# Optimization experiments

Measured on AMD Instinct MI355X. Metric: run time of the kernel, lower is better.

## Reference

```python
import jax, jax.numpy as jnp
import numpy as np

E = 1024
H = 16
D = E // H
S = 2048
B = 2

def setup_inputs() -> dict:
    key = jax.random.key(0)
    ks = jax.random.split(key, 5)
    x = jax.random.normal(ks[0], (B, S, E), dtype=jnp.float32)
    W_qkv = jax.random.normal(ks[1], (E, 3 * E), dtype=jnp.float32) / np.sqrt(E)
    b_qkv = jax.random.normal(ks[2], (3 * E,), dtype=jnp.float32) * 0.02
    W_out = jax.random.normal(ks[3], (E, E), dtype=jnp.float32) / np.sqrt(E)
    b_out = jax.random.normal(ks[4], (E,), dtype=jnp.float32) * 0.02
    return {"x": x, "W_qkv": W_qkv, "b_qkv": b_qkv, "W_out": W_out, "b_out": b_out}

def reference(x, W_qkv, b_qkv, W_out, b_out):
    b, s, e = x.shape
    qkv = x @ W_qkv + b_qkv                      # [B,S,3E]
    q, k, v = jnp.split(qkv, 3, axis=-1)
    # [B,S,E] -> [B,H,S,D]
    q = q.reshape(b, s, H, D).transpose(0, 2, 1, 3)
    k = k.reshape(b, s, H, D).transpose(0, 2, 1, 3)
    v = v.reshape(b, s, H, D).transpose(0, 2, 1, 3)
    scale = 1.0 / np.sqrt(D)
    att = jnp.einsum('bhqd,bhkd->bhqk', q, k) * scale
    causal = jnp.tril(jnp.ones((s, s), dtype=bool))
    att = jnp.where(causal[None, None], att, -jnp.inf)
    att = jax.nn.softmax(att, axis=-1)
    out = jnp.einsum('bhqk,bhkd->bhqd', att, v)  # [B,H,S,D]
    out = out.transpose(0, 2, 1, 3).reshape(b, s, e)
    return out @ W_out + b_out
```

## Files before the change

kernel.cpp:

```cpp
#include <hip/hip_runtime.h>

typedef unsigned short u16;
typedef __bf16  bf16x8 __attribute__((ext_vector_type(8)));
typedef float   f32x4  __attribute__((ext_vector_type(4)));
typedef unsigned int   u32x4 __attribute__((ext_vector_type(4)));
typedef unsigned short u16x4 __attribute__((ext_vector_type(4)));
typedef unsigned short u16x8 __attribute__((ext_vector_type(8)));

#define BB 2
#define HH 16
#define DD 64
#define SS 2048
#define EE 1024

#define QSCALE 0.1803368801111244f

static __device__ __forceinline__ u16 f2bf(float f) {
    unsigned int u = __float_as_uint(f);
    u += 0x7FFFu + ((u >> 16) & 1u);
    return (u16)(u >> 16);
}

union BfCast { u32x4 u; bf16x8 b; };
static __device__ __forceinline__ bf16x8 ldb8(const u16* p) {
    BfCast x; x.u = *(const u32x4*)p; return x.b;
}

static __device__ __forceinline__ void gload16(const u16* g, u16* l) {
    __builtin_amdgcn_global_load_lds(
        (const __attribute__((address_space(1))) unsigned int*)g,
        (__attribute__((address_space(3))) unsigned int*)l, 16, 0, 0);
}

#define UG (32 * 512)
static __device__ __forceinline__ int kidx(int s, int d) {
    return (((s >> 4) * 2 + (d >> 5)) * 512) + ((((d >> 3) & 3) * 16 + (s & 15)) * 8) + (d & 7);
}
static __device__ __forceinline__ int vidx(int key, int d) {
    return (((key >> 5) * 4 + (d >> 4)) * 512) + ((((key >> 3) & 3) * 16 + (d & 15)) * 8) + (key & 7);
}

__global__ __launch_bounds__(256) void prep_kernel(
    const float* __restrict__ x,    u16* __restrict__ xb,
    const float* __restrict__ Wqkv, u16* __restrict__ wqkvT,
    const float* __restrict__ Wout, u16* __restrict__ woutT)
{
    __shared__ float tile[32][33];
    const int bid = blockIdx.x;
    if (bid < 2048) {
        const int t = bid * 256 + threadIdx.x;
        const int u = t >> 6, w = t & 63;
        const int m = (u >> 5) * 16 + (w & 15);
        const int k = (u & 31) * 32 + (w >> 4) * 8;
        const float* p = x + m * 1024 + k;
        const f32x4 a = *(const f32x4*)p;
        const f32x4 b = *(const f32x4*)(p + 4);
        u16x8 o;
        o[0] = f2bf(a[0]); o[1] = f2bf(a[1]); o[2] = f2bf(a[2]); o[3] = f2bf(a[3]);
        o[4] = f2bf(b[0]); o[5] = f2bf(b[1]); o[6] = f2bf(b[2]); o[7] = f2bf(b[3]);
        *(u16x8*)&xb[u * 512 + w * 8] = o;
        return;
    }
    const float* in; u16* out; int C, tb;
    if (bid < 2048 + 3072) { in = Wqkv; out = wqkvT; C = 3072; tb = bid - 2048; }
    else                   { in = Wout; out = woutT; C = 1024; tb = bid - 5120; }
    const int tx = threadIdx.x & 31;
    const int ty = threadIdx.x >> 5;
    const int ct = C >> 5;
    const int bc = tb % ct, br = tb / ct;
    const int c0 = bc * 32, r0 = br * 32;
    #pragma unroll
    for (int i = 0; i < 4; i++)
        tile[ty + i * 8][tx] = in[(r0 + ty + i * 8) * C + c0 + tx];
    __syncthreads();
    #pragma unroll
    for (int i = 0; i < 4; i++) {
        const int n = c0 + ty + i * 8;
        out[((n >> 4) * 32 + (r0 >> 5)) * 512 + (((tx >> 3) & 3) * 16 + (n & 15)) * 8 + (tx & 7)]
            = f2bf(tile[tx][ty + i * 8]);
    }
}

__global__ __launch_bounds__(256) void gemm_qkv_kernel(
    const u16* __restrict__ Af,
    const u16* __restrict__ Bf,
    const float* __restrict__ bias,
    u16* __restrict__ Qb, u16* __restrict__ Kb, u16* __restrict__ Vb)
{
    __shared__ __align__(16) u16 Us[2][16 * 512];
    const int lane = threadIdx.x & 63;
    const int wave = threadIdx.x >> 6;
    const int nb = 3 * EE / 128;
    const int tm = blockIdx.x / nb, tn = blockIdx.x % nb;
    const int lm = lane & 15, quad = lane >> 4;

    const u16* sp[4];
    #pragma unroll
    for (int j = 0; j < 4; j++) {
        const int idx = 4 * wave + j;
        sp[j] = (idx < 8) ? (Af + (tm * 8 + idx) * UG + lane * 8)
                          : (Bf + (tn * 8 + idx - 8) * UG + lane * 8);
    }
    u16* ld0 = &Us[0][4 * wave * 512];
    u16* ld1 = &Us[1][4 * wave * 512];

    const int wy = wave >> 1, wx = wave & 1;
    f32x4 acc[4][4] = {};

    #pragma unroll
    for (int j = 0; j < 4; j++) gload16(sp[j], ld0 + j * 512);

    for (int it = 0; it < 32; ++it) {
        const int cur = it & 1;
        __syncthreads();
        if (it + 1 < 32) {
            u16* ld = cur ? ld0 : ld1;
            const int ko = (it + 1) * 512;
            #pragma unroll
            for (int j = 0; j < 4; j++) gload16(sp[j] + ko, ld + j * 512);
        }
        bf16x8 af[4], bf[4];
        #pragma unroll
        for (int i = 0; i < 4; i++) {
            af[i] = ldb8(&Us[cur][(wy * 4 + i) * 512 + lane * 8]);
            bf[i] = ldb8(&Us[cur][(8 + wx * 4 + i) * 512 + lane * 8]);
        }
        #pragma unroll
        for (int mi = 0; mi < 4; mi++)
            #pragma unroll
            for (int ni = 0; ni < 4; ni++)
                acc[mi][ni] = __builtin_amdgcn_mfma_f32_16x16x32_bf16(af[mi], bf[ni], acc[mi][ni], 0, 0, 0);
    }

    const int gm0 = tm * 128 + wy * 64;
    const int gn0 = tn * 128 + wx * 64;
    #pragma unroll
    for (int ni = 0; ni < 4; ni++) {
        const int n = gn0 + ni * 16 + lm;
        const float bv = bias[n];
        const int which = n >> 10;
        const int e = n & 1023;
        const int h = e >> 6, d = e & 63;
        #pragma unroll
        for (int mi = 0; mi < 4; mi++) {
            if (which == 2) {
                const int m0 = gm0 + mi * 16 + quad * 4;
                const int b = m0 >> 11, key0 = m0 & 2047;
                u16x4 pk;
                #pragma unroll
                for (int r = 0; r < 4; r++) pk[r] = f2bf(acc[mi][ni][r] + bv);
                *(u16x4*)&Vb[(b * HH + h) * 131072 + vidx(key0, d)] = pk;
            } else if (which == 1) {
                #pragma unroll
                for (int r = 0; r < 4; r++) {
                    const int m = gm0 + mi * 16 + quad * 4 + r;
                    const int b = m >> 11, s = m & 2047;
                    Kb[(b * HH + h) * 131072 + kidx(s, d)] = f2bf(acc[mi][ni][r] + bv);
                }
            } else {
                #pragma unroll
                for (int r = 0; r < 4; r++) {
                    const int m = gm0 + mi * 16 + quad * 4 + r;
                    const int b = m >> 11, s = m & 2047;
                    Qb[((b * HH + h) * SS + s) * DD + d] = f2bf((acc[mi][ni][r] + bv) * QSCALE);
                }
            }
        }
    }
}

__global__ __launch_bounds__(256) void attn_kernel(
    const u16* __restrict__ Qb, const u16* __restrict__ Kb,
    const u16* __restrict__ Vb, u16* __restrict__ Ob)
{
    __shared__ __align__(16) u16 Ks[2][4096];
    __shared__ __align__(16) u16 Vs[2][4096];
    __shared__ __align__(16) u16 Plds[4 * 16 * 72];
    const int tid = threadIdx.x;
    const int lane = tid & 63, wave = tid >> 6;
    const int lm = lane & 15, quad = lane >> 4;
    const int bh = blockIdx.x & 31;
    const int qt = (SS / 64 - 1) - (blockIdx.x >> 5);
    const int q0 = qt * 64;
    const int qrow = q0 + wave * 16;
    const int b = bh >> 4, h = bh & 15;

    const u16* qbase = Qb + (bh * SS + qrow) * DD;
    const bf16x8 qf0 = ldb8(qbase + lm * DD + quad * 8);
    const bf16x8 qf1 = ldb8(qbase + lm * DD + 32 + quad * 8);

    const u16* ktile = Kb + bh * 131072;
    const u16* vtile = Vb + bh * 131072;
    u16* Pw = Plds + wave * (16 * 72);

    BfCast oc; oc.u = (u32x4){0x3F803F80u, 0x3F803F80u, 0x3F803F80u, 0x3F803F80u};
    const bf16x8 ones = oc.b;

    f32x4 oacc[4] = {};
    f32x4 lacc = {0.f, 0.f, 0.f, 0.f};

    const int ktmax = qt + 1;
    {
        const u16* kg = ktile + wave * 1024 + lane * 8;
        const u16* vg = vtile + wave * 1024 + lane * 8;
        gload16(kg,       &Ks[0][wave * 1024]);
        gload16(kg + 512, &Ks[0][wave * 1024 + 512]);
        gload16(vg,       &Vs[0][wave * 1024]);
        gload16(vg + 512, &Vs[0][wave * 1024 + 512]);
    }
    for (int kt = 0; kt < ktmax; ++kt) {
        const int cur = kt & 1;
        const int k0 = kt * 64;
        __syncthreads();
        if (kt + 1 < ktmax) {
            const u16* kg = ktile + (kt + 1) * 4096 + wave * 1024 + lane * 8;
            const u16* vg = vtile + (kt + 1) * 4096 + wave * 1024 + lane * 8;
            gload16(kg,       &Ks[cur ^ 1][wave * 1024]);
            gload16(kg + 512, &Ks[cur ^ 1][wave * 1024 + 512]);
            gload16(vg,       &Vs[cur ^ 1][wave * 1024]);
            gload16(vg + 512, &Vs[cur ^ 1][wave * 1024 + 512]);
        }

        f32x4 s[4];
        #pragma unroll
        for (int g = 0; g < 4; g++) {
            f32x4 z = {0.f, 0.f, 0.f, 0.f};
            z    = __builtin_amdgcn_mfma_f32_16x16x32_bf16(ldb8(&Ks[cur][(g * 2) * 512 + lane * 8]), qf0, z, 0, 0, 0);
            s[g] = __builtin_amdgcn_mfma_f32_16x16x32_bf16(ldb8(&Ks[cur][(g * 2 + 1) * 512 + lane * 8]), qf1, z, 0, 0, 0);
        }
        if (k0 + 63 > qrow) {
            const int lim = qrow + lm - k0 - quad * 4;
            #pragma unroll
            for (int g = 0; g < 4; g++)
                #pragma unroll
                for (int r = 0; r < 4; r++)
                    if (g * 16 + r > lim) s[g][r] = -INFINITY;
        }
        #pragma unroll
        for (int g = 0; g < 4; g++) {
            u16x4 pk;
            #pragma unroll
            for (int r = 0; r < 4; r++) pk[r] = f2bf(__builtin_amdgcn_exp2f(s[g][r]));
            *(u16x4*)&Pw[lm * 72 + g * 16 + quad * 4] = pk;
        }
        const bf16x8 pf0 = ldb8(&Pw[lm * 72 + quad * 8]);
        const bf16x8 pf1 = ldb8(&Pw[lm * 72 + 32 + quad * 8]);
        lacc = __builtin_amdgcn_mfma_f32_16x16x32_bf16(ones, pf0, lacc, 0, 0, 0);
        lacc = __builtin_amdgcn_mfma_f32_16x16x32_bf16(ones, pf1, lacc, 0, 0, 0);
        #pragma unroll
        for (int dg = 0; dg < 4; dg++) {
            oacc[dg] = __builtin_amdgcn_mfma_f32_16x16x32_bf16(ldb8(&Vs[cur][dg * 512 + lane * 8]), pf0, oacc[dg], 0, 0, 0);
            oacc[dg] = __builtin_amdgcn_mfma_f32_16x16x32_bf16(ldb8(&Vs[cur][(4 + dg) * 512 + lane * 8]), pf1, oacc[dg], 0, 0, 0);
        }
    }
    const float inv = 1.0f / lacc[0];
    u16* ob = Ob + (((b * SS + qrow) >> 4) * 32 + h * 2) * 512;
    #pragma unroll
    for (int dg = 0; dg < 4; dg++) {
        u16x4 pk;
        #pragma unroll
        for (int r = 0; r < 4; r++) pk[r] = f2bf(oacc[dg][r] * inv);
        *(u16x4*)&ob[(dg >> 1) * 512 + (((dg * 2 + (quad >> 1)) & 3) * 16 + lm) * 8 + (quad & 1) * 4] = pk;
    }
}

__global__ __launch_bounds__(256) void gemm_out_kernel(
    const u16* __restrict__ Af,
    const u16* __restrict__ Bf,
    const float* __restrict__ bias,
    float* __restrict__ Out)
{
    __shared__ __align__(16) u16 Us[2][16 * 512];
    const int lane = threadIdx.x & 63;
    const int wave = threadIdx.x >> 6;
    const int nb = EE / 128;
    const int tm = blockIdx.x / nb, tn = blockIdx.x % nb;
    const int lm = lane & 15, quad = lane >> 4;

    const u16* sp[4];
    #pragma unroll
    for (int j = 0; j < 4; j++) {
        const int idx = 4 * wave + j;
        sp[j] = (idx < 8) ? (Af + (tm * 8 + idx) * UG + lane * 8)
                          : (Bf + (tn * 8 + idx - 8) * UG + lane * 8);
    }
    u16* ld0 = &Us[0][4 * wave * 512];
    u16* ld1 = &Us[1][4 * wave * 512];

    const int wy = wave >> 1, wx = wave & 1;
    f32x4 acc[4][4] = {};

    #pragma unroll
    for (int j = 0; j < 4; j++) gload16(sp[j], ld0 + j * 512);

    for (int it = 0; it < 32; ++it) {
        const int cur = it & 1;
        __syncthreads();
        if (it + 1 < 32) {
            u16* ld = cur ? ld0 : ld1;
            const int ko = (it + 1) * 512;
            #pragma unroll
            for (int j = 0; j < 4; j++) gload16(sp[j] + ko, ld + j * 512);
        }
        bf16x8 af[4], bf[4];
        #pragma unroll
        for (int i = 0; i < 4; i++) {
            af[i] = ldb8(&Us[cur][(wy * 4 + i) * 512 + lane * 8]);
            bf[i] = ldb8(&Us[cur][(8 + wx * 4 + i) * 512 + lane * 8]);
        }
        #pragma unroll
        for (int mi = 0; mi < 4; mi++)
            #pragma unroll
            for (int ni = 0; ni < 4; ni++)
                acc[mi][ni] = __builtin_amdgcn_mfma_f32_16x16x32_bf16(af[mi], bf[ni], acc[mi][ni], 0, 0, 0);
    }

    const int gm0 = tm * 128 + wy * 64;
    const int gn0 = tn * 128 + wx * 64;
    #pragma unroll
    for (int ni = 0; ni < 4; ni++) {
        const int n = gn0 + ni * 16 + lm;
        const float bv = bias[n];
        #pragma unroll
        for (int mi = 0; mi < 4; mi++)
            #pragma unroll
            for (int r = 0; r < 4; r++)
                Out[(gm0 + mi * 16 + quad * 4 + r) * EE + n] = acc[mi][ni][r] + bv;
    }
}

extern "C" void kernel_launch(void* const* d_in, const int* in_sizes, int n_in,
                              void* d_out, int out_size, void* d_ws, size_t ws_size,
                              hipStream_t stream)
{
    const float* x     = (const float*)d_in[0];
    const float* Wqkv  = (const float*)d_in[1];
    const float* bqkv  = (const float*)d_in[2];
    const float* Wout  = (const float*)d_in[3];
    const float* bout  = (const float*)d_in[4];
    float* out = (float*)d_out;

    char* ws = (char*)d_ws;
    u16* xb    = (u16*)(ws + 0);
    u16* wqkvT = (u16*)(ws + 8388608);
    u16* woutT = (u16*)(ws + 14680064);
    u16* Qb    = (u16*)(ws + 16777216);
    u16* Kb    = (u16*)(ws + 25165824);
    u16* Vb    = (u16*)(ws + 33554432);
    u16* Ob    = (u16*)(ws + 41943040);
    if (ws_size < 50331648) return;

    prep_kernel<<<2048 + 3072 + 1024, 256, 0, stream>>>(x, xb, Wqkv, wqkvT, Wout, woutT);
    gemm_qkv_kernel<<<(BB * SS / 128) * (3 * EE / 128), 256, 0, stream>>>(xb, wqkvT, bqkv, Qb, Kb, Vb);
    attn_kernel<<<BB * HH * (SS / 64), 256, 0, stream>>>(Qb, Kb, Vb, Ob);
    gemm_out_kernel<<<(BB * SS / 128) * (EE / 128), 256, 0, stream>>>(Ob, woutT, bout, out);
}
```

Measured before the change: 171.9 us.

## Process 128 query rows per attention block, two 16-row fragments per wave

The attention kernel now gives each block 128 query rows instead of 64. Each wave owns 32 rows as two 16-row fragments that share the same K/V tiles staged in LDS. This halves the grid and the total global K/V traffic per query, and amortizes LDS loads and barriers over more compute. In exchange it uses more registers and launches fewer blocks (512), which may hurt occupancy and load balance on the causal triangle. Fully masked fragments are skipped per key tile.

```diff
diff --git a/kernel.cpp b/kernel.cpp
--- a/kernel.cpp
+++ b/kernel.cpp
@@ -180,14 +180,18 @@
     const int lane = tid & 63, wave = tid >> 6;
     const int lm = lane & 15, quad = lane >> 4;
     const int bh = blockIdx.x & 31;
-    const int qt = (SS / 64 - 1) - (blockIdx.x >> 5);
-    const int q0 = qt * 64;
-    const int qrow = q0 + wave * 16;
+    const int qt = (SS / 128 - 1) - (blockIdx.x >> 5);
+    const int q0 = qt * 128;
+    const int qrow = q0 + wave * 32;
     const int b = bh >> 4, h = bh & 15;
 
     const u16* qbase = Qb + (bh * SS + qrow) * DD;
-    const bf16x8 qf0 = ldb8(qbase + lm * DD + quad * 8);
-    const bf16x8 qf1 = ldb8(qbase + lm * DD + 32 + quad * 8);
+    bf16x8 qf[2][2];
+    #pragma unroll
+    for (int f = 0; f < 2; f++) {
+        qf[f][0] = ldb8(qbase + (f * 16 + lm) * DD + quad * 8);
+        qf[f][1] = ldb8(qbase + (f * 16 + lm) * DD + 32 + quad * 8);
+    }
 
     const u16* ktile = Kb + bh * 131072;
     const u16* vtile = Vb + bh * 131072;
@@ -196,10 +200,10 @@
     BfCast oc; oc.u = (u32x4){0x3F803F80u, 0x3F803F80u, 0x3F803F80u, 0x3F803F80u};
     const bf16x8 ones = oc.b;
 
-    f32x4 oacc[4] = {};
-    f32x4 lacc = {0.f, 0.f, 0.f, 0.f};
-
-    const int ktmax = qt + 1;
+    f32x4 oacc[2][4] = {};
+    f32x4 lacc[2] = {};
+
+    const int ktmax = qt * 2 + 2;
     {
         const u16* kg = ktile + wave * 1024 + lane * 8;
         const u16* vg = vtile + wave * 1024 + lane * 8;
@@ -221,46 +225,55 @@
             gload16(vg + 512, &Vs[cur ^ 1][wave * 1024 + 512]);
         }
 
-        f32x4 s[4];
-        #pragma unroll
-        for (int g = 0; g < 4; g++) {
-            f32x4 z = {0.f, 0.f, 0.f, 0.f};
-            z    = __builtin_amdgcn_mfma_f32_16x16x32_bf16(ldb8(&Ks[cur][(g * 2) * 512 + lane * 8]), qf0, z, 0, 0, 0);
-            s[g] = __builtin_amdgcn_mfma_f32_16x16x32_bf16(ldb8(&Ks[cur][(g * 2 + 1) * 512 + lane * 8]), qf1, z, 0, 0, 0);
-        }
-        if (k0 + 63 > qrow) {
-            const int lim = qrow + lm - k0 - quad * 4;
-            #pragma unroll
-            for (int g = 0; g < 4; g++)
-                #pragma unroll
-                for (int r = 0; r < 4; r++)
-                    if (g * 16 + r > lim) s[g][r] = -INFINITY;
-        }
-        #pragma unroll
-        for (int g = 0; g < 4; g++) {
+        #pragma unroll
+        for (int f = 0; f < 2; f++) {
+            const int qrf = qrow + f * 16;
+            if (k0 > qrf + 15) continue;
+
+            f32x4 s[4];
+            #pragma unroll
+            for (int g = 0; g < 4; g++) {
+                f32x4 z = {0.f, 0.f, 0.f, 0.f};
+                z    = __builtin_amdgcn_mfma_f32_16x16x32_bf16(ldb8(&Ks[cur][(g * 2) * 512 + lane * 8]), qf[f][0], z, 0, 0, 0);
+                s[g] = __builtin_amdgcn_mfma_f32_16x16x32_bf16(ldb8(&Ks[cur][(g * 2 + 1) * 512 + lane * 8]), qf[f][1], z, 0, 0, 0);
+            }
+            if (k0 + 63 > qrf) {
+                const int lim = qrf + lm - k0 - quad * 4;
+                #pragma unroll
+                for (int g = 0; g < 4; g++)
+                    #pragma unroll
+                    for (int r = 0; r < 4; r++)
+                        if (g * 16 + r > lim) s[g][r] = -INFINITY;
+            }
+            #pragma unroll
+            for (int g = 0; g < 4; g++) {
+                u16x4 pk;
+                #pragma unroll
+                for (int r = 0; r < 4; r++) pk[r] = f2bf(__builtin_amdgcn_exp2f(s[g][r]));
+                *(u16x4*)&Pw[lm * 72 + g * 16 + quad * 4] = pk;
+            }
+            const bf16x8 pf0 = ldb8(&Pw[lm * 72 + quad * 8]);
+            const bf16x8 pf1 = ldb8(&Pw[lm * 72 + 32 + quad * 8]);
+            lacc[f] = __builtin_amdgcn_mfma_f32_16x16x32_bf16(ones, pf0, lacc[f], 0, 0, 0);
+            lacc[f] = __builtin_amdgcn_mfma_f32_16x16x32_bf16(ones, pf1, lacc[f], 0, 0, 0);
+            #pragma unroll
+            for (int dg = 0; dg < 4; dg++) {
+                oacc[f][dg] = __builtin_amdgcn_mfma_f32_16x16x32_bf16(ldb8(&Vs[cur][dg * 512 + lane * 8]), pf0, oacc[f][dg], 0, 0, 0);
+                oacc[f][dg] = __builtin_amdgcn_mfma_f32_16x16x32_bf16(ldb8(&Vs[cur][(4 + dg) * 512 + lane * 8]), pf1, oacc[f][dg], 0, 0, 0);
+            }
+        }
+    }
+    #pragma unroll
+    for (int f = 0; f < 2; f++) {
+        const float inv = 1.0f / lacc[f][0];
+        u16* ob = Ob + (((b * SS + qrow + f * 16) >> 4) * 32 + h * 2) * 512;
+        #pragma unroll
+        for (int dg = 0; dg < 4; dg++) {
             u16x4 pk;
             #pragma unroll
-            for (int r = 0; r < 4; r++) pk[r] = f2bf(__builtin_amdgcn_exp2f(s[g][r]));
-            *(u16x4*)&Pw[lm * 72 + g * 16 + quad * 4] = pk;
-        }
-        const bf16x8 pf0 = ldb8(&Pw[lm * 72 + quad * 8]);
-        const bf16x8 pf1 = ldb8(&Pw[lm * 72 + 32 + quad * 8]);
-        lacc = __builtin_amdgcn_mfma_f32_16x16x32_bf16(ones, pf0, lacc, 0, 0, 0);
-        lacc = __builtin_amdgcn_mfma_f32_16x16x32_bf16(ones, pf1, lacc, 0, 0, 0);
-        #pragma unroll
-        for (int dg = 0; dg < 4; dg++) {
-            oacc[dg] = __builtin_amdgcn_mfma_f32_16x16x32_bf16(ldb8(&Vs[cur][dg * 512 + lane * 8]), pf0, oacc[dg], 0, 0, 0);
-            oacc[dg] = __builtin_amdgcn_mfma_f32_16x16x32_bf16(ldb8(&Vs[cur][(4 + dg) * 512 + lane * 8]), pf1, oacc[dg], 0, 0, 0);
-        }
-    }
-    const float inv = 1.0f / lacc[0];
-    u16* ob = Ob + (((b * SS + qrow) >> 4) * 32 + h * 2) * 512;
-    #pragma unroll
-    for (int dg = 0; dg < 4; dg++) {
-        u16x4 pk;
-        #pragma unroll
-        for (int r = 0; r < 4; r++) pk[r] = f2bf(oacc[dg][r] * inv);
-        *(u16x4*)&ob[(dg >> 1) * 512 + (((dg * 2 + (quad >> 1)) & 3) * 16 + lm) * 8 + (quad & 1) * 4] = pk;
+            for (int r = 0; r < 4; r++) pk[r] = f2bf(oacc[f][dg][r] * inv);
+            *(u16x4*)&ob[(dg >> 1) * 512 + (((dg * 2 + (quad >> 1)) & 3) * 16 + lm) * 8 + (quad & 1) * 4] = pk;
+        }
     }
 }
 
@@ -352,6 +365,6 @@
 
     prep_kernel<<<2048 + 3072 + 1024, 256, 0, stream>>>(x, xb, Wqkv, wqkvT, Wout, woutT);
     gemm_qkv_kernel<<<(BB * SS / 128) * (3 * EE / 128), 256, 0, stream>>>(xb, wqkvT, bqkv, Qb, Kb, Vb);
-    attn_kernel<<<BB * HH * (SS / 64), 256, 0, stream>>>(Qb, Kb, Vb, Ob);
+    attn_kernel<<<BB * HH * (SS / 128), 256, 0, stream>>>(Qb, Kb, Vb, Ob);
     gemm_out_kernel<<<(BB * SS / 128) * (EE / 128), 256, 0, stream>>>(Ob, woutT, bout, out);
 }
```

Measured after the change: 188.0 us. 9.4% more time.

## Pair mirrored causal query tiles per 512-thread attention block, use packed bf16 cvt

Applied to the files above, without the earlier changes.

Each attention block now runs 8 waves and handles two query tiles, qt and 31-qt. Both tiles share one K/V staging stream, which balances causal work across blocks and halves the block count. Waves on the shorter tile skip compute once past their diagonal but still take part in loads and barriers. The software bf16 rounding is also replaced with the v_cvt_pk_bf16_f32 instruction for P and output packing.

```diff
diff --git a/kernel.cpp b/kernel.cpp
--- a/kernel.cpp
+++ b/kernel.cpp
@@ -3,6 +3,7 @@
 typedef unsigned short u16;
 typedef __bf16  bf16x8 __attribute__((ext_vector_type(8)));
 typedef float   f32x4  __attribute__((ext_vector_type(4)));
+typedef unsigned int   u32x2 __attribute__((ext_vector_type(2)));
 typedef unsigned int   u32x4 __attribute__((ext_vector_type(4)));
 typedef unsigned short u16x4 __attribute__((ext_vector_type(4)));
 typedef unsigned short u16x8 __attribute__((ext_vector_type(8)));
@@ -19,6 +20,12 @@
     unsigned int u = __float_as_uint(f);
     u += 0x7FFFu + ((u >> 16) & 1u);
     return (u16)(u >> 16);
+}
+
+static __device__ __forceinline__ unsigned int cvtpk(float lo, float hi) {
+    unsigned int r;
+    asm("v_cvt_pk_bf16_f32 %0, %1, %2" : "=v"(r) : "v"(lo), "v"(hi));
+    return r;
 }
 
 union BfCast { u32x4 u; bf16x8 b; };
@@ -169,20 +176,21 @@
     }
 }
 
-__global__ __launch_bounds__(256) void attn_kernel(
+__global__ __launch_bounds__(512) void attn_kernel(
     const u16* __restrict__ Qb, const u16* __restrict__ Kb,
     const u16* __restrict__ Vb, u16* __restrict__ Ob)
 {
     __shared__ __align__(16) u16 Ks[2][4096];
     __shared__ __align__(16) u16 Vs[2][4096];
-    __shared__ __align__(16) u16 Plds[4 * 16 * 72];
+    __shared__ __align__(16) u16 Plds[8 * 16 * 72];
     const int tid = threadIdx.x;
     const int lane = tid & 63, wave = tid >> 6;
     const int lm = lane & 15, quad = lane >> 4;
     const int bh = blockIdx.x & 31;
-    const int qt = (SS / 64 - 1) - (blockIdx.x >> 5);
-    const int q0 = qt * 64;
-    const int qrow = q0 + wave * 16;
+    const int pr = blockIdx.x >> 5;
+    const int qtA = 31 - pr, qtB = pr;
+    const int qt_w = (wave < 4) ? qtA : qtB;
+    const int qrow = qt_w * 64 + (wave & 3) * 16;
     const int b = bh >> 4, h = bh & 15;
 
     const u16* qbase = Qb + (bh * SS + qrow) * DD;
@@ -199,68 +207,62 @@
     f32x4 oacc[4] = {};
     f32x4 lacc = {0.f, 0.f, 0.f, 0.f};
 
-    const int ktmax = qt + 1;
+    const int ktmax = qtA + 1;
     {
-        const u16* kg = ktile + wave * 1024 + lane * 8;
-        const u16* vg = vtile + wave * 1024 + lane * 8;
-        gload16(kg,       &Ks[0][wave * 1024]);
-        gload16(kg + 512, &Ks[0][wave * 1024 + 512]);
-        gload16(vg,       &Vs[0][wave * 1024]);
-        gload16(vg + 512, &Vs[0][wave * 1024 + 512]);
+        gload16(ktile + wave * 512 + lane * 8, &Ks[0][wave * 512]);
+        gload16(vtile + wave * 512 + lane * 8, &Vs[0][wave * 512]);
     }
     for (int kt = 0; kt < ktmax; ++kt) {
         const int cur = kt & 1;
         const int k0 = kt * 64;
         __syncthreads();
         if (kt + 1 < ktmax) {
-            const u16* kg = ktile + (kt + 1) * 4096 + wave * 1024 + lane * 8;
-            const u16* vg = vtile + (kt + 1) * 4096 + wave * 1024 + lane * 8;
-            gload16(kg,       &Ks[cur ^ 1][wave * 1024]);
-            gload16(kg + 512, &Ks[cur ^ 1][wave * 1024 + 512]);
-            gload16(vg,       &Vs[cur ^ 1][wave * 1024]);
-            gload16(vg + 512, &Vs[cur ^ 1][wave * 1024 + 512]);
-        }
-
-        f32x4 s[4];
-        #pragma unroll
-        for (int g = 0; g < 4; g++) {
-            f32x4 z = {0.f, 0.f, 0.f, 0.f};
-            z    = __builtin_amdgcn_mfma_f32_16x16x32_bf16(ldb8(&Ks[cur][(g * 2) * 512 + lane * 8]), qf0, z, 0, 0, 0);
-            s[g] = __builtin_amdgcn_mfma_f32_16x16x32_bf16(ldb8(&Ks[cur][(g * 2 + 1) * 512 + lane * 8]), qf1, z, 0, 0, 0);
-        }
-        if (k0 + 63 > qrow) {
-            const int lim = qrow + lm - k0 - quad * 4;
-            #pragma unroll
-            for (int g = 0; g < 4; g++)
+            gload16(ktile + (kt + 1) * 4096 + wave * 512 + lane * 8, &Ks[cur ^ 1][wave * 512]);
+            gload16(vtile + (kt + 1) * 4096 + wave * 512 + lane * 8, &Vs[cur ^ 1][wave * 512]);
+        }
+
+        if (kt <= qt_w) {
+            f32x4 s[4];
+            #pragma unroll
+            for (int g = 0; g < 4; g++) {
+                f32x4 z = {0.f, 0.f, 0.f, 0.f};
+                z    = __builtin_amdgcn_mfma_f32_16x16x32_bf16(ldb8(&Ks[cur][(g * 2) * 512 + lane * 8]), qf0, z, 0, 0, 0);
+                s[g] = __builtin_amdgcn_mfma_f32_16x16x32_bf16(ldb8(&Ks[cur][(g * 2 + 1) * 512 + lane * 8]), qf1, z, 0, 0, 0);
+            }
+            if (k0 + 63 > qrow) {
+                const int lim = qrow + lm - k0 - quad * 4;
                 #pragma unroll
-                for (int r = 0; r < 4; r++)
-                    if (g * 16 + r > lim) s[g][r] = -INFINITY;
-        }
-        #pragma unroll
-        for (int g = 0; g < 4; g++) {
-            u16x4 pk;
-            #pragma unroll
-            for (int r = 0; r < 4; r++) pk[r] = f2bf(__builtin_amdgcn_exp2f(s[g][r]));
-            *(u16x4*)&Pw[lm * 72 + g * 16 + quad * 4] = pk;
-        }
-        const bf16x8 pf0 = ldb8(&Pw[lm * 72 + quad * 8]);
-        const bf16x8 pf1 = ldb8(&Pw[lm * 72 + 32 + quad * 8]);
-        lacc = __builtin_amdgcn_mfma_f32_16x16x32_bf16(ones, pf0, lacc, 0, 0, 0);
-        lacc = __builtin_amdgcn_mfma_f32_16x16x32_bf16(ones, pf1, lacc, 0, 0, 0);
-        #pragma unroll
-        for (int dg = 0; dg < 4; dg++) {
-            oacc[dg] = __builtin_amdgcn_mfma_f32_16x16x32_bf16(ldb8(&Vs[cur][dg * 512 + lane * 8]), pf0, oacc[dg], 0, 0, 0);
-            oacc[dg] = __builtin_amdgcn_mfma_f32_16x16x32_bf16(ldb8(&Vs[cur][(4 + dg) * 512 + lane * 8]), pf1, oacc[dg], 0, 0, 0);
+                for (int g = 0; g < 4; g++)
+                    #pragma unroll
+                    for (int r = 0; r < 4; r++)
+                        if (g * 16 + r > lim) s[g][r] = -INFINITY;
+            }
+            #pragma unroll
+            for (int g = 0; g < 4; g++) {
+                u32x2 w;
+                w[0] = cvtpk(__builtin_amdgcn_exp2f(s[g][0]), __builtin_amdgcn_exp2f(s[g][1]));
+                w[1] = cvtpk(__builtin_amdgcn_exp2f(s[g][2]), __builtin_amdgcn_exp2f(s[g][3]));
+                *(u32x2*)&Pw[lm * 72 + g * 16 + quad * 4] = w;
+            }
+            const bf16x8 pf0 = ldb8(&Pw[lm * 72 + quad * 8]);
+            const bf16x8 pf1 = ldb8(&Pw[lm * 72 + 32 + quad * 8]);
+            lacc = __builtin_amdgcn_mfma_f32_16x16x32_bf16(ones, pf0, lacc, 0, 0, 0);
+            lacc = __builtin_amdgcn_mfma_f32_16x16x32_bf16(ones, pf1, lacc, 0, 0, 0);
+            #pragma unroll
+            for (int dg = 0; dg < 4; dg++) {
+                oacc[dg] = __builtin_amdgcn_mfma_f32_16x16x32_bf16(ldb8(&Vs[cur][dg * 512 + lane * 8]), pf0, oacc[dg], 0, 0, 0);
+                oacc[dg] = __builtin_amdgcn_mfma_f32_16x16x32_bf16(ldb8(&Vs[cur][(4 + dg) * 512 + lane * 8]), pf1, oacc[dg], 0, 0, 0);
+            }
         }
     }
     const float inv = 1.0f / lacc[0];
     u16* ob = Ob + (((b * SS + qrow) >> 4) * 32 + h * 2) * 512;
     #pragma unroll
     for (int dg = 0; dg < 4; dg++) {
-        u16x4 pk;
-        #pragma unroll
-        for (int r = 0; r < 4; r++) pk[r] = f2bf(oacc[dg][r] * inv);
-        *(u16x4*)&ob[(dg >> 1) * 512 + (((dg * 2 + (quad >> 1)) & 3) * 16 + lm) * 8 + (quad & 1) * 4] = pk;
+        u32x2 w;
+        w[0] = cvtpk(oacc[dg][0] * inv, oacc[dg][1] * inv);
+        w[1] = cvtpk(oacc[dg][2] * inv, oacc[dg][3] * inv);
+        *(u32x2*)&ob[(dg >> 1) * 512 + (((dg * 2 + (quad >> 1)) & 3) * 16 + lm) * 8 + (quad & 1) * 4] = w;
     }
 }
 
@@ -352,6 +354,6 @@
 
     prep_kernel<<<2048 + 3072 + 1024, 256, 0, stream>>>(x, xb, Wqkv, wqkvT, Wout, woutT);
     gemm_qkv_kernel<<<(BB * SS / 128) * (3 * EE / 128), 256, 0, stream>>>(xb, wqkvT, bqkv, Qb, Kb, Vb);
-    attn_kernel<<<BB * HH * (SS / 64), 256, 0, stream>>>(Qb, Kb, Vb, Ob);
+    attn_kernel<<<BB * HH * (SS / 128), 512, 0, stream>>>(Qb, Kb, Vb, Ob);
     gemm_out_kernel<<<(BB * SS / 128) * (EE / 128), 256, 0, stream>>>(Ob, woutT, bout, out);
 }
```

Result: no change. 171.8 us (-0.1%).
